# Performance work log

Hardware: AMD Instinct MI355X
Metric: run time of the kernel (lower is better)

Reference implementation:

```python
import jax, jax.numpy as jnp
import numpy as np

N_NODES = 100_000
N_EDGES = 3_200_000
IN_DIM, HID_DIM, EMB_DIM = 128, 64, 32


def setup_inputs() -> dict:
    key = jax.random.key(0)
    k0, k1, k2, k3, k4, k5 = jax.random.split(key, 6)
    x = jax.random.normal(k0, (N_NODES, IN_DIM), dtype=jnp.float32)
    edge_index = jax.random.randint(k1, (2, N_EDGES), 0, N_NODES, dtype=jnp.int32)
    # GCNConv parameters (glorot-ish scale)
    W1 = jax.random.normal(k2, (IN_DIM, HID_DIM), dtype=jnp.float32) / np.sqrt(IN_DIM)
    b1 = jnp.zeros((HID_DIM,), dtype=jnp.float32)
    W2 = jax.random.normal(k3, (HID_DIM, EMB_DIM), dtype=jnp.float32) / np.sqrt(HID_DIM)
    b2 = jnp.zeros((EMB_DIM,), dtype=jnp.float32)
    return {"x": x, "W1": W1, "b1": b1, "W2": W2, "b2": b2, "edge_index": edge_index}


def reference(x, W1, b1, W2, b2, edge_index):
    """Two-layer GCN encoder (PyG GCNConv semantics, eval mode so dropout is a no-op).

    Each GCNConv: add self-loops, symmetric deg^-1/2 normalization,
    out = scatter_add(norm_e * (x @ W)[src], dst) + b.
    """
    N = x.shape[0]
    loops = jnp.arange(N, dtype=edge_index.dtype)
    src = jnp.concatenate([edge_index[0], loops])  # [E+N]
    dst = jnp.concatenate([edge_index[1], loops])  # [E+N]

    # degree of destination nodes (self-loops guarantee deg >= 1)
    deg = jax.ops.segment_sum(jnp.ones_like(dst, dtype=jnp.float32), dst,
                              num_segments=N)
    dinv = jax.lax.rsqrt(deg)                      # deg^-1/2, finite since deg>=1
    norm = dinv[src] * dinv[dst]                   # [E+N]

    def gcn_conv(h, W, b):
        h = h @ W                                  # dense transform [N, D_out]
        msg = h[src] * norm[:, None]               # gather + scale [E+N, D_out]
        return jax.ops.segment_sum(msg, dst, num_segments=N) + b

    h = jax.nn.relu(gcn_conv(x, W1, b1))
    # F.dropout with training=False is identity -> omitted
    return gcn_conv(h, W2, b2)
```

## Files before the change

### kernel.cpp

```cpp
#include <hip/hip_runtime.h>

static constexpr int NN = 100000;
static constexpr int NE = 3200000;
static constexpr int DI = 128;
static constexpr int DH = 64;
static constexpr int DO = 32;

static constexpr int NBK  = 391;
static constexpr int BCAP = 9216;
static constexpr int TILE = 8192;

typedef short short8 __attribute__((ext_vector_type(8)));
typedef float f32x4  __attribute__((ext_vector_type(4)));

__device__ __forceinline__ unsigned short f2bf(float f) {
    union { float f; unsigned u; } v; v.f = f;
    unsigned r = v.u + 0x7FFFu + ((v.u >> 16) & 1u);
    return (unsigned short)(r >> 16);
}
__device__ __forceinline__ float bflo(unsigned u) {
    union { unsigned u; float f; } v; v.u = u << 16; return v.f;
}
__device__ __forceinline__ float bfhi(unsigned u) {
    union { unsigned u; float f; } v; v.u = u & 0xFFFF0000u; return v.f;
}

__global__ void k_zero(int* __restrict__ p, int n) {
    int i = blockIdx.x * blockDim.x + threadIdx.x;
    if (i < n) p[i] = 0;
}

__global__ __launch_bounds__(256) void k_bucket(
        const int* __restrict__ src, const int* __restrict__ dst,
        int* __restrict__ bcur, int* __restrict__ bstore) {
    __shared__ int hist[NBK];
    __shared__ int lcur[NBK];
    __shared__ int gpos[NBK];
    __shared__ int stage[TILE];
    __shared__ unsigned short bid[TILE];

    int tid = threadIdx.x;
    for (int i = tid; i < NBK; i += 256) hist[i] = 0;
    __syncthreads();

    int base = blockIdx.x * TILE;
    int p[32]; unsigned short bb[32];
#pragma unroll
    for (int k = 0; k < 32; ++k) {
        int e = base + k * 256 + tid;
        if (e < NE) {
            int d = dst[e], s = src[e];
            bb[k] = (unsigned short)(d >> 8);
            p[k]  = ((d & 255) << 24) | s;
            atomicAdd(&hist[bb[k]], 1);
        } else bb[k] = 0xFFFF;
    }
    __syncthreads();

    for (int i = tid; i < NBK; i += 256)
        gpos[i] = atomicAdd(&bcur[i], hist[i]);
    __syncthreads();

    if (tid < 64) {
        int carry = 0;
        for (int c = 0; c < (NBK + 63) / 64; ++c) {
            int idx = c * 64 + tid;
            int v = (idx < NBK) ? hist[idx] : 0;
            int inc = v;
#pragma unroll
            for (int o = 1; o < 64; o <<= 1) {
                int u = __shfl_up(inc, o, 64);
                if (tid >= o) inc += u;
            }
            int tot = __shfl(inc, 63, 64);
            if (idx < NBK) { int ex = carry + inc - v; hist[idx] = ex; lcur[idx] = ex; }
            carry += tot;
        }
    }
    __syncthreads();

#pragma unroll
    for (int k = 0; k < 32; ++k) {
        if (bb[k] != 0xFFFF) {
            int lp = atomicAdd(&lcur[bb[k]], 1);
            stage[lp] = p[k];
            bid[lp] = bb[k];
        }
    }
    __syncthreads();

    int tcnt = min(TILE, NE - base);
    for (int i = tid; i < tcnt; i += 256) {
        int b = bid[i];
        int off = gpos[b] + (i - hist[b]);
        if (off < BCAP) bstore[b * BCAP + off] = stage[i];
    }
}

__global__ __launch_bounds__(256) void k_bsort(
        const int* __restrict__ bcur, int* __restrict__ bstore,
        int* __restrict__ rpb, int* __restrict__ rpe, float* __restrict__ dinv) {
    __shared__ int buf[BCAP];
    __shared__ int sorted[BCAP];
    __shared__ int hist[256], scan[256], cur[256];

    int b = blockIdx.x, tid = threadIdx.x;
    int cnt = min(bcur[b], BCAP);
    int base = b * BCAP;
    for (int i = tid; i < cnt; i += 256) buf[i] = bstore[base + i];
    hist[tid] = 0;
    __syncthreads();
    for (int i = tid; i < cnt; i += 256)
        atomicAdd(&hist[((unsigned)buf[i]) >> 24], 1);
    __syncthreads();

    if (tid < 64) {
        int carry = 0;
        for (int c = 0; c < 4; ++c) {
            int idx = c * 64 + tid;
            int v = hist[idx];
            int inc = v;
#pragma unroll
            for (int o = 1; o < 64; o <<= 1) {
                int u = __shfl_up(inc, o, 64);
                if (tid >= o) inc += u;
            }
            int tot = __shfl(inc, 63, 64);
            scan[idx] = carry + inc - v;
            cur[idx]  = carry + inc - v;
            carry += tot;
        }
    }
    __syncthreads();

    int n = b * 256 + tid;
    if (n < NN) {
        int beg = base + scan[tid];
        rpb[n] = beg;
        rpe[n] = beg + hist[tid];
        dinv[n] = rsqrtf(1.0f + (float)hist[tid]);
    }

    for (int i = tid; i < cnt; i += 256) {
        unsigned pv = (unsigned)buf[i];
        int pos = atomicAdd(&cur[pv >> 24], 1);
        sorted[pos] = (int)(pv & 0xFFFFFF);
    }
    __syncthreads();
    for (int i = tid; i < cnt; i += 256) bstore[base + i] = sorted[i];
}

__global__ __launch_bounds__(256) void k_cast_x(const float* __restrict__ x,
                                                unsigned* __restrict__ xbf32) {
    int i = blockIdx.x * 256 + threadIdx.x;
    float a = x[(size_t)i * 4 + 0], b = x[(size_t)i * 4 + 1];
    float c = x[(size_t)i * 4 + 2], d = x[(size_t)i * 4 + 3];
    xbf32[(size_t)i * 2 + 0] = (unsigned)f2bf(a) | ((unsigned)f2bf(b) << 16);
    xbf32[(size_t)i * 2 + 1] = (unsigned)f2bf(c) | ((unsigned)f2bf(d) << 16);
}

__global__ __launch_bounds__(256) void k_cast_w(const float* __restrict__ W1,
                                                const float* __restrict__ W2,
                                                unsigned short* __restrict__ w1bf,
                                                unsigned short* __restrict__ w2bf) {
    int tid = threadIdx.x;
    for (int i = tid; i < DI * DH; i += 256) w1bf[i] = f2bf(W1[i]);
    for (int i = tid; i < DH * DO; i += 256) w2bf[i] = f2bf(W2[i]);
}

__global__ __launch_bounds__(256) void k_xw1_mfma(
        const unsigned short* __restrict__ xbf, const unsigned short* __restrict__ w1bf,
        const float* __restrict__ dinv, unsigned short* __restrict__ h1b) {
    int wave = threadIdx.x >> 6, lane = threadIdx.x & 63;
    int q = lane >> 4, m = lane & 15, o0 = wave * 16;
    int nb = blockIdx.x * 64;

    short8 bf[4];
#pragma unroll
    for (int kb = 0; kb < 4; ++kb)
#pragma unroll
        for (int j = 0; j < 8; ++j)
            bf[kb][j] = (short)w1bf[(kb * 32 + q * 8 + j) * DH + o0 + m];

#pragma unroll
    for (int mt = 0; mt < 4; ++mt) {
        int row = nb + mt * 16 + m;
        f32x4 acc = {0.f, 0.f, 0.f, 0.f};
#pragma unroll
        for (int kb = 0; kb < 4; ++kb) {
            short8 a = *(const short8*)(xbf + (size_t)row * DI + kb * 32 + q * 8);
            acc = __builtin_amdgcn_mfma_f32_16x16x32_bf16(a, bf[kb], acc, 0, 0, 0);
        }
#pragma unroll
        for (int r = 0; r < 4; ++r) {
            int n = nb + mt * 16 + q * 4 + r;
            if (n < NN) h1b[(size_t)n * DH + o0 + m] = f2bf(acc[r] * dinv[n]);
        }
    }
}

__global__ __launch_bounds__(256) void k_gather64(
        const int* __restrict__ rpb, const int* __restrict__ rpe,
        const int* __restrict__ csr, const unsigned* __restrict__ h,
        const float* __restrict__ dinv, const float* __restrict__ b1,
        unsigned* __restrict__ tbf) {
    int wave = threadIdx.x >> 6, lane = threadIdx.x & 63;
    int q = lane >> 4, f4 = lane & 15;
    int n = blockIdx.x * 4 + wave;
    int beg = rpb[n], end = rpe[n];

    float s0 = 0.f, s1 = 0.f, s2 = 0.f, s3 = 0.f;
    if (q == 0) {
        uint2 u = *(const uint2*)(h + (size_t)n * 32 + 2 * f4);
        s0 = bflo(u.x); s1 = bfhi(u.x); s2 = bflo(u.y); s3 = bfhi(u.y);
    }
    for (int c = beg; c < end; c += 64) {
        int cnt = min(64, end - c);
        int sidx = (lane < cnt) ? csr[c + lane] : 0;
        int j = 0;
        for (; j + 8 <= cnt; j += 8) {
            int sa = __shfl(sidx, j + q, 64);
            int sb = __shfl(sidx, j + 4 + q, 64);
            uint2 ua = *(const uint2*)(h + (size_t)sa * 32 + 2 * f4);
            uint2 ub = *(const uint2*)(h + (size_t)sb * 32 + 2 * f4);
            s0 += bflo(ua.x); s1 += bfhi(ua.x); s2 += bflo(ua.y); s3 += bfhi(ua.y);
            s0 += bflo(ub.x); s1 += bfhi(ub.x); s2 += bflo(ub.y); s3 += bfhi(ub.y);
        }
        for (; j < cnt; j += 4) {
            int slot = j + q;
            int s = __shfl(sidx, slot, 64);
            if (slot < cnt) {
                uint2 u = *(const uint2*)(h + (size_t)s * 32 + 2 * f4);
                s0 += bflo(u.x); s1 += bfhi(u.x); s2 += bflo(u.y); s3 += bfhi(u.y);
            }
        }
    }
    s0 += __shfl_xor(s0, 32, 64); s1 += __shfl_xor(s1, 32, 64);
    s2 += __shfl_xor(s2, 32, 64); s3 += __shfl_xor(s3, 32, 64);
    s0 += __shfl_xor(s0, 16, 64); s1 += __shfl_xor(s1, 16, 64);
    s2 += __shfl_xor(s2, 16, 64); s3 += __shfl_xor(s3, 16, 64);
    if (q == 0) {
        float dn = dinv[n];
        float t0 = fmaxf(fmaf(s0, dn, b1[4 * f4 + 0]), 0.f);
        float t1 = fmaxf(fmaf(s1, dn, b1[4 * f4 + 1]), 0.f);
        float t2 = fmaxf(fmaf(s2, dn, b1[4 * f4 + 2]), 0.f);
        float t3 = fmaxf(fmaf(s3, dn, b1[4 * f4 + 3]), 0.f);
        uint2 o;
        o.x = (unsigned)f2bf(t0) | ((unsigned)f2bf(t1) << 16);
        o.y = (unsigned)f2bf(t2) | ((unsigned)f2bf(t3) << 16);
        *(uint2*)(tbf + (size_t)n * 32 + 2 * f4) = o;
    }
}

__global__ __launch_bounds__(256) void k_l2_mfma(
        const unsigned short* __restrict__ tbf, const unsigned short* __restrict__ w2bf,
        const float* __restrict__ dinv, unsigned short* __restrict__ h2b) {
    int wave = threadIdx.x >> 6, lane = threadIdx.x & 63;
    int q = lane >> 4, m = lane & 15;
    int o0 = (wave & 1) * 16, mt = wave >> 1;
    int nb = blockIdx.x * 32;

    short8 bf[2];
#pragma unroll
    for (int kb = 0; kb < 2; ++kb)
#pragma unroll
        for (int j = 0; j < 8; ++j)
            bf[kb][j] = (short)w2bf[(kb * 32 + q * 8 + j) * DO + o0 + m];

    int row = nb + mt * 16 + m;
    f32x4 acc = {0.f, 0.f, 0.f, 0.f};
#pragma unroll
    for (int kb = 0; kb < 2; ++kb) {
        short8 a = *(const short8*)(tbf + (size_t)row * DH + kb * 32 + q * 8);
        acc = __builtin_amdgcn_mfma_f32_16x16x32_bf16(a, bf[kb], acc, 0, 0, 0);
    }
#pragma unroll
    for (int r = 0; r < 4; ++r) {
        int n = nb + mt * 16 + q * 4 + r;
        if (n < NN) h2b[(size_t)n * DO + o0 + m] = f2bf(acc[r] * dinv[n]);
    }
}

__global__ __launch_bounds__(256) void k_gather32(
        const int* __restrict__ rpb, const int* __restrict__ rpe,
        const int* __restrict__ csr, const unsigned* __restrict__ h,
        const float* __restrict__ dinv, const float* __restrict__ b2,
        float* __restrict__ out) {
    int wave = threadIdx.x >> 6, lane = threadIdx.x & 63;
    int q = lane >> 3, f4 = lane & 7;
    int n = blockIdx.x * 4 + wave;
    int beg = rpb[n], end = rpe[n];

    float s0 = 0.f, s1 = 0.f, s2 = 0.f, s3 = 0.f;
    if (q == 0) {
        uint2 u = *(const uint2*)(h + (size_t)n * 16 + 2 * f4);
        s0 = bflo(u.x); s1 = bfhi(u.x); s2 = bflo(u.y); s3 = bfhi(u.y);
    }
    for (int c = beg; c < end; c += 64) {
        int cnt = min(64, end - c);
        int sidx = (lane < cnt) ? csr[c + lane] : 0;
        int j = 0;
        for (; j + 16 <= cnt; j += 16) {
            int sa = __shfl(sidx, j + q, 64);
            int sb = __shfl(sidx, j + 8 + q, 64);
            uint2 ua = *(const uint2*)(h + (size_t)sa * 16 + 2 * f4);
            uint2 ub = *(const uint2*)(h + (size_t)sb * 16 + 2 * f4);
            s0 += bflo(ua.x); s1 += bfhi(ua.x); s2 += bflo(ua.y); s3 += bfhi(ua.y);
            s0 += bflo(ub.x); s1 += bfhi(ub.x); s2 += bflo(ub.y); s3 += bfhi(ub.y);
        }
        for (; j < cnt; j += 8) {
            int slot = j + q;
            int s = __shfl(sidx, slot, 64);
            if (slot < cnt) {
                uint2 u = *(const uint2*)(h + (size_t)s * 16 + 2 * f4);
                s0 += bflo(u.x); s1 += bfhi(u.x); s2 += bflo(u.y); s3 += bfhi(u.y);
            }
        }
    }
    s0 += __shfl_xor(s0, 32, 64); s1 += __shfl_xor(s1, 32, 64);
    s2 += __shfl_xor(s2, 32, 64); s3 += __shfl_xor(s3, 32, 64);
    s0 += __shfl_xor(s0, 16, 64); s1 += __shfl_xor(s1, 16, 64);
    s2 += __shfl_xor(s2, 16, 64); s3 += __shfl_xor(s3, 16, 64);
    s0 += __shfl_xor(s0, 8, 64);  s1 += __shfl_xor(s1, 8, 64);
    s2 += __shfl_xor(s2, 8, 64);  s3 += __shfl_xor(s3, 8, 64);
    if (q == 0) {
        float dn = dinv[n];
        size_t o = (size_t)n * 32 + 4 * f4;
        out[o + 0] = fmaf(s0, dn, b2[4 * f4 + 0]);
        out[o + 1] = fmaf(s1, dn, b2[4 * f4 + 1]);
        out[o + 2] = fmaf(s2, dn, b2[4 * f4 + 2]);
        out[o + 3] = fmaf(s3, dn, b2[4 * f4 + 3]);
    }
}

extern "C" void kernel_launch(void* const* d_in, const int* in_sizes, int n_in,
                              void* d_out, int out_size, void* d_ws, size_t ws_size,
                              hipStream_t stream) {
    const float* x  = (const float*)d_in[0];
    const float* W1 = (const float*)d_in[1];
    const float* b1 = (const float*)d_in[2];
    const float* W2 = (const float*)d_in[3];
    const float* b2 = (const float*)d_in[4];
    const int* ei  = (const int*)d_in[5];
    const int* src = ei;
    const int* dst = ei + NE;
    float* out = (float*)d_out;

    float* ws    = (float*)d_ws;
    int*   rpb   = (int*)ws;
    int*   rpe   = (int*)(ws + 100352);
    float* dinv  = ws + 200704;
    int*   bcur  = (int*)(ws + 301056);
    int*   bstor = (int*)(ws + 301568);
    unsigned short* w1bf = (unsigned short*)(ws + 3905024);
    unsigned short* w2bf = (unsigned short*)(ws + 3909120);
    unsigned short* xbf  = (unsigned short*)(ws + 3910144);
    unsigned short* tbf  = xbf;
    unsigned short* h1b  = (unsigned short*)(ws + 10332672);
    unsigned short* h2b  = h1b;

    k_zero     <<<2, 256, 0, stream>>>(bcur, 512);
    k_bucket   <<<(NE + TILE - 1) / TILE, 256, 0, stream>>>(src, dst, bcur, bstor);
    k_bsort    <<<NBK, 256, 0, stream>>>(bcur, bstor, rpb, rpe, dinv);

    k_cast_x   <<<NN * DI / 4 / 256, 256, 0, stream>>>(x, (unsigned*)xbf);
    k_cast_w   <<<1, 256, 0, stream>>>(W1, W2, w1bf, w2bf);

    k_xw1_mfma <<<(NN + 63) / 64, 256, 0, stream>>>(xbf, w1bf, dinv, h1b);
    k_gather64 <<<NN / 4, 256, 0, stream>>>(rpb, rpe, bstor, (const unsigned*)h1b,
                                            dinv, b1, (unsigned*)tbf);
    k_l2_mfma  <<<NN / 32, 256, 0, stream>>>(tbf, w2bf, dinv, h2b);
    k_gather32 <<<NN / 4, 256, 0, stream>>>(rpb, rpe, bstor, (const unsigned*)h2b,
                                            dinv, b2, out);
}
```

Before: 295.1 us.

## Fuse bucketing, weight cast and X·W1 into one launch; scale by dinv in gather

Merges the edge bucketing kernel, the W2 cast, and the X·W1 MFMA (now reading fp32 x and W1 directly and converting in registers) into a single heterogeneous launch. This removes the separate x-cast pass and its bf16 round trip through memory, and lets the matmul overlap with bucketing. Because dinv is not yet known when h1 is computed, the source-side dinv scaling moves into the layer-1 gather as an extra per-edge dinv load. k_bsort also goes to 512 threads per block. The cost is an extra random 4-byte load per edge in the gather and larger shared-memory blocks running alongside the matmul blocks.

Measured after the change: 274.7 us. -6.9%, faster.

```diff
diff --git a/kernel.cpp b/kernel.cpp
--- a/kernel.cpp
+++ b/kernel.cpp
@@ -9,6 +9,8 @@
 static constexpr int NBK  = 391;
 static constexpr int BCAP = 9216;
 static constexpr int TILE = 8192;
+static constexpr int XW1_BASE = 392;
+static constexpr int XW1_BLOCKS = (NN + 63) / 64;
 
 typedef short short8 __attribute__((ext_vector_type(8)));
 typedef float f32x4  __attribute__((ext_vector_type(4)));
@@ -30,9 +32,12 @@
     if (i < n) p[i] = 0;
 }
 
-__global__ __launch_bounds__(256) void k_bucket(
+__global__ __launch_bounds__(256) void k_mega(
         const int* __restrict__ src, const int* __restrict__ dst,
-        int* __restrict__ bcur, int* __restrict__ bstore) {
+        int* __restrict__ bcur, int* __restrict__ bstore,
+        const float* __restrict__ x, const float* __restrict__ W1,
+        const float* __restrict__ W2,
+        unsigned short* __restrict__ w2bf, unsigned short* __restrict__ h1b) {
     __shared__ int hist[NBK];
     __shared__ int lcur[NBK];
     __shared__ int gpos[NBK];
@@ -40,64 +45,103 @@
     __shared__ unsigned short bid[TILE];
 
     int tid = threadIdx.x;
-    for (int i = tid; i < NBK; i += 256) hist[i] = 0;
-    __syncthreads();
-
-    int base = blockIdx.x * TILE;
-    int p[32]; unsigned short bb[32];
-#pragma unroll
-    for (int k = 0; k < 32; ++k) {
-        int e = base + k * 256 + tid;
-        if (e < NE) {
-            int d = dst[e], s = src[e];
-            bb[k] = (unsigned short)(d >> 8);
-            p[k]  = ((d & 255) << 24) | s;
-            atomicAdd(&hist[bb[k]], 1);
-        } else bb[k] = 0xFFFF;
-    }
-    __syncthreads();
-
-    for (int i = tid; i < NBK; i += 256)
-        gpos[i] = atomicAdd(&bcur[i], hist[i]);
-    __syncthreads();
-
-    if (tid < 64) {
-        int carry = 0;
-        for (int c = 0; c < (NBK + 63) / 64; ++c) {
-            int idx = c * 64 + tid;
-            int v = (idx < NBK) ? hist[idx] : 0;
-            int inc = v;
-#pragma unroll
-            for (int o = 1; o < 64; o <<= 1) {
-                int u = __shfl_up(inc, o, 64);
-                if (tid >= o) inc += u;
-            }
-            int tot = __shfl(inc, 63, 64);
-            if (idx < NBK) { int ex = carry + inc - v; hist[idx] = ex; lcur[idx] = ex; }
-            carry += tot;
-        }
-    }
-    __syncthreads();
-
-#pragma unroll
-    for (int k = 0; k < 32; ++k) {
-        if (bb[k] != 0xFFFF) {
-            int lp = atomicAdd(&lcur[bb[k]], 1);
-            stage[lp] = p[k];
-            bid[lp] = bb[k];
-        }
-    }
-    __syncthreads();
-
-    int tcnt = min(TILE, NE - base);
-    for (int i = tid; i < tcnt; i += 256) {
-        int b = bid[i];
-        int off = gpos[b] + (i - hist[b]);
-        if (off < BCAP) bstore[b * BCAP + off] = stage[i];
-    }
-}
-
-__global__ __launch_bounds__(256) void k_bsort(
+
+    if (blockIdx.x < NBK) {
+        for (int i = tid; i < NBK; i += 256) hist[i] = 0;
+        __syncthreads();
+
+        int base = blockIdx.x * TILE;
+        int p[32]; unsigned short bb[32];
+#pragma unroll
+        for (int k = 0; k < 32; ++k) {
+            int e = base + k * 256 + tid;
+            if (e < NE) {
+                int d = dst[e], s = src[e];
+                bb[k] = (unsigned short)(d >> 8);
+                p[k]  = ((d & 255) << 24) | s;
+                atomicAdd(&hist[bb[k]], 1);
+            } else bb[k] = 0xFFFF;
+        }
+        __syncthreads();
+
+        for (int i = tid; i < NBK; i += 256)
+            gpos[i] = atomicAdd(&bcur[i], hist[i]);
+        __syncthreads();
+
+        if (tid < 64) {
+            int carry = 0;
+            for (int c = 0; c < (NBK + 63) / 64; ++c) {
+                int idx = c * 64 + tid;
+                int v = (idx < NBK) ? hist[idx] : 0;
+                int inc = v;
+#pragma unroll
+                for (int o = 1; o < 64; o <<= 1) {
+                    int u = __shfl_up(inc, o, 64);
+                    if (tid >= o) inc += u;
+                }
+                int tot = __shfl(inc, 63, 64);
+                if (idx < NBK) { int ex = carry + inc - v; hist[idx] = ex; lcur[idx] = ex; }
+                carry += tot;
+            }
+        }
+        __syncthreads();
+
+#pragma unroll
+        for (int k = 0; k < 32; ++k) {
+            if (bb[k] != 0xFFFF) {
+                int lp = atomicAdd(&lcur[bb[k]], 1);
+                stage[lp] = p[k];
+                bid[lp] = bb[k];
+            }
+        }
+        __syncthreads();
+
+        int tcnt = min(TILE, NE - base);
+        for (int i = tid; i < tcnt; i += 256) {
+            int b = bid[i];
+            int off = gpos[b] + (i - hist[b]);
+            if (off < BCAP) bstore[b * BCAP + off] = stage[i];
+        }
+    } else if (blockIdx.x == NBK) {
+        for (int i = tid; i < DH * DO; i += 256) w2bf[i] = f2bf(W2[i]);
+    } else {
+        int wave = tid >> 6, lane = tid & 63;
+        int q = lane >> 4, m = lane & 15, o0 = wave * 16;
+        int nb = (blockIdx.x - XW1_BASE) * 64;
+
+        short8 bfr[4];
+#pragma unroll
+        for (int kb = 0; kb < 4; ++kb)
+#pragma unroll
+            for (int j = 0; j < 8; ++j)
+                bfr[kb][j] = (short)f2bf(W1[(kb * 32 + q * 8 + j) * DH + o0 + m]);
+
+#pragma unroll
+        for (int mt = 0; mt < 4; ++mt) {
+            int row = min(nb + mt * 16 + m, NN - 1);
+            const float* xr = x + (size_t)row * DI;
+            f32x4 acc = {0.f, 0.f, 0.f, 0.f};
+#pragma unroll
+            for (int kb = 0; kb < 4; ++kb) {
+                f32x4 u0 = *(const f32x4*)(xr + kb * 32 + q * 8);
+                f32x4 u1 = *(const f32x4*)(xr + kb * 32 + q * 8 + 4);
+                short8 a;
+                a[0] = (short)f2bf(u0.x); a[1] = (short)f2bf(u0.y);
+                a[2] = (short)f2bf(u0.z); a[3] = (short)f2bf(u0.w);
+                a[4] = (short)f2bf(u1.x); a[5] = (short)f2bf(u1.y);
+                a[6] = (short)f2bf(u1.z); a[7] = (short)f2bf(u1.w);
+                acc = __builtin_amdgcn_mfma_f32_16x16x32_bf16(a, bfr[kb], acc, 0, 0, 0);
+            }
+#pragma unroll
+            for (int r = 0; r < 4; ++r) {
+                int n = nb + mt * 16 + q * 4 + r;
+                if (n < NN) h1b[(size_t)n * DH + o0 + m] = f2bf(acc[r]);
+            }
+        }
+    }
+}
+
+__global__ __launch_bounds__(512) void k_bsort(
         const int* __restrict__ bcur, int* __restrict__ bstore,
         int* __restrict__ rpb, int* __restrict__ rpe, float* __restrict__ dinv) {
     __shared__ int buf[BCAP];
@@ -107,10 +151,10 @@
     int b = blockIdx.x, tid = threadIdx.x;
     int cnt = min(bcur[b], BCAP);
     int base = b * BCAP;
-    for (int i = tid; i < cnt; i += 256) buf[i] = bstore[base + i];
-    hist[tid] = 0;
+    for (int i = tid; i < cnt; i += 512) buf[i] = bstore[base + i];
+    if (tid < 256) hist[tid] = 0;
     __syncthreads();
-    for (int i = tid; i < cnt; i += 256)
+    for (int i = tid; i < cnt; i += 512)
         atomicAdd(&hist[((unsigned)buf[i]) >> 24], 1);
     __syncthreads();
 
@@ -133,70 +177,23 @@
     }
     __syncthreads();
 
-    int n = b * 256 + tid;
-    if (n < NN) {
-        int beg = base + scan[tid];
-        rpb[n] = beg;
-        rpe[n] = beg + hist[tid];
-        dinv[n] = rsqrtf(1.0f + (float)hist[tid]);
-    }
-
-    for (int i = tid; i < cnt; i += 256) {
+    if (tid < 256) {
+        int n = b * 256 + tid;
+        if (n < NN) {
+            int beg = base + scan[tid];
+            rpb[n] = beg;
+            rpe[n] = beg + hist[tid];
+            dinv[n] = rsqrtf(1.0f + (float)hist[tid]);
+        }
+    }
+
+    for (int i = tid; i < cnt; i += 512) {
         unsigned pv = (unsigned)buf[i];
         int pos = atomicAdd(&cur[pv >> 24], 1);
         sorted[pos] = (int)(pv & 0xFFFFFF);
     }
     __syncthreads();
-    for (int i = tid; i < cnt; i += 256) bstore[base + i] = sorted[i];
-}
-
-__global__ __launch_bounds__(256) void k_cast_x(const float* __restrict__ x,
-                                                unsigned* __restrict__ xbf32) {
-    int i = blockIdx.x * 256 + threadIdx.x;
-    float a = x[(size_t)i * 4 + 0], b = x[(size_t)i * 4 + 1];
-    float c = x[(size_t)i * 4 + 2], d = x[(size_t)i * 4 + 3];
-    xbf32[(size_t)i * 2 + 0] = (unsigned)f2bf(a) | ((unsigned)f2bf(b) << 16);
-    xbf32[(size_t)i * 2 + 1] = (unsigned)f2bf(c) | ((unsigned)f2bf(d) << 16);
-}
-
-__global__ __launch_bounds__(256) void k_cast_w(const float* __restrict__ W1,
-                                                const float* __restrict__ W2,
-                                                unsigned short* __restrict__ w1bf,
-                                                unsigned short* __restrict__ w2bf) {
-    int tid = threadIdx.x;
-    for (int i = tid; i < DI * DH; i += 256) w1bf[i] = f2bf(W1[i]);
-    for (int i = tid; i < DH * DO; i += 256) w2bf[i] = f2bf(W2[i]);
-}
-
-__global__ __launch_bounds__(256) void k_xw1_mfma(
-        const unsigned short* __restrict__ xbf, const unsigned short* __restrict__ w1bf,
-        const float* __restrict__ dinv, unsigned short* __restrict__ h1b) {
-    int wave = threadIdx.x >> 6, lane = threadIdx.x & 63;
-    int q = lane >> 4, m = lane & 15, o0 = wave * 16;
-    int nb = blockIdx.x * 64;
-
-    short8 bf[4];
-#pragma unroll
-    for (int kb = 0; kb < 4; ++kb)
-#pragma unroll
-        for (int j = 0; j < 8; ++j)
-            bf[kb][j] = (short)w1bf[(kb * 32 + q * 8 + j) * DH + o0 + m];
-
-#pragma unroll
-    for (int mt = 0; mt < 4; ++mt) {
-        int row = nb + mt * 16 + m;
-        f32x4 acc = {0.f, 0.f, 0.f, 0.f};
-#pragma unroll
-        for (int kb = 0; kb < 4; ++kb) {
-            short8 a = *(const short8*)(xbf + (size_t)row * DI + kb * 32 + q * 8);
-            acc = __builtin_amdgcn_mfma_f32_16x16x32_bf16(a, bf[kb], acc, 0, 0, 0);
-        }
-#pragma unroll
-        for (int r = 0; r < 4; ++r) {
-            int n = nb + mt * 16 + q * 4 + r;
-            if (n < NN) h1b[(size_t)n * DH + o0 + m] = f2bf(acc[r] * dinv[n]);
-        }
-    }
+    for (int i = tid; i < cnt; i += 512) bstore[base + i] = sorted[i];
 }
 
 __global__ __launch_bounds__(256) void k_gather64(
@@ -208,11 +205,13 @@
     int q = lane >> 4, f4 = lane & 15;
     int n = blockIdx.x * 4 + wave;
     int beg = rpb[n], end = rpe[n];
+    float dn = dinv[n];
 
     float s0 = 0.f, s1 = 0.f, s2 = 0.f, s3 = 0.f;
     if (q == 0) {
         uint2 u = *(const uint2*)(h + (size_t)n * 32 + 2 * f4);
-        s0 = bflo(u.x); s1 = bfhi(u.x); s2 = bflo(u.y); s3 = bfhi(u.y);
+        s0 = bflo(u.x) * dn; s1 = bfhi(u.x) * dn;
+        s2 = bflo(u.y) * dn; s3 = bfhi(u.y) * dn;
     }
     for (int c = beg; c < end; c += 64) {
         int cnt = min(64, end - c);
@@ -221,17 +220,22 @@
         for (; j + 8 <= cnt; j += 8) {
             int sa = __shfl(sidx, j + q, 64);
             int sb = __shfl(sidx, j + 4 + q, 64);
+            float da = dinv[sa], db = dinv[sb];
             uint2 ua = *(const uint2*)(h + (size_t)sa * 32 + 2 * f4);
             uint2 ub = *(const uint2*)(h + (size_t)sb * 32 + 2 * f4);
-            s0 += bflo(ua.x); s1 += bfhi(ua.x); s2 += bflo(ua.y); s3 += bfhi(ua.y);
-            s0 += bflo(ub.x); s1 += bfhi(ub.x); s2 += bflo(ub.y); s3 += bfhi(ub.y);
+            s0 = fmaf(bflo(ua.x), da, s0); s1 = fmaf(bfhi(ua.x), da, s1);
+            s2 = fmaf(bflo(ua.y), da, s2); s3 = fmaf(bfhi(ua.y), da, s3);
+            s0 = fmaf(bflo(ub.x), db, s0); s1 = fmaf(bfhi(ub.x), db, s1);
+            s2 = fmaf(bflo(ub.y), db, s2); s3 = fmaf(bfhi(ub.y), db, s3);
         }
         for (; j < cnt; j += 4) {
             int slot = j + q;
             int s = __shfl(sidx, slot, 64);
             if (slot < cnt) {
+                float dv = dinv[s];
                 uint2 u = *(const uint2*)(h + (size_t)s * 32 + 2 * f4);
-                s0 += bflo(u.x); s1 += bfhi(u.x); s2 += bflo(u.y); s3 += bfhi(u.y);
+                s0 = fmaf(bflo(u.x), dv, s0); s1 = fmaf(bfhi(u.x), dv, s1);
+                s2 = fmaf(bflo(u.y), dv, s2); s3 = fmaf(bfhi(u.y), dv, s3);
             }
         }
     }
@@ -240,7 +244,6 @@
     s0 += __shfl_xor(s0, 16, 64); s1 += __shfl_xor(s1, 16, 64);
     s2 += __shfl_xor(s2, 16, 64); s3 += __shfl_xor(s3, 16, 64);
     if (q == 0) {
-        float dn = dinv[n];
         float t0 = fmaxf(fmaf(s0, dn, b1[4 * f4 + 0]), 0.f);
         float t1 = fmaxf(fmaf(s1, dn, b1[4 * f4 + 1]), 0.f);
         float t2 = fmaxf(fmaf(s2, dn, b1[4 * f4 + 2]), 0.f);
@@ -352,21 +355,16 @@
     float* dinv  = ws + 200704;
     int*   bcur  = (int*)(ws + 301056);
     int*   bstor = (int*)(ws + 301568);
-    unsigned short* w1bf = (unsigned short*)(ws + 3905024);
-    unsigned short* w2bf = (unsigned short*)(ws + 3909120);
-    unsigned short* xbf  = (unsigned short*)(ws + 3910144);
-    unsigned short* tbf  = xbf;
-    unsigned short* h1b  = (unsigned short*)(ws + 10332672);
+    unsigned short* w2bf = (unsigned short*)(ws + 3905024);
+    unsigned short* tbf  = (unsigned short*)(ws + 3906048);
+    unsigned short* h1b  = (unsigned short*)(ws + 7106048);
     unsigned short* h2b  = h1b;
 
     k_zero     <<<2, 256, 0, stream>>>(bcur, 512);
-    k_bucket   <<<(NE + TILE - 1) / TILE, 256, 0, stream>>>(src, dst, bcur, bstor);
-    k_bsort    <<<NBK, 256, 0, stream>>>(bcur, bstor, rpb, rpe, dinv);
-
-    k_cast_x   <<<NN * DI / 4 / 256, 256, 0, stream>>>(x, (unsigned*)xbf);
-    k_cast_w   <<<1, 256, 0, stream>>>(W1, W2, w1bf, w2bf);
-
-    k_xw1_mfma <<<(NN + 63) / 64, 256, 0, stream>>>(xbf, w1bf, dinv, h1b);
+    k_mega     <<<XW1_BASE + XW1_BLOCKS, 256, 0, stream>>>(
+                    src, dst, bcur, bstor, x, W1, W2, w2bf, h1b);
+    k_bsort    <<<NBK, 512, 0, stream>>>(bcur, bstor, rpb, rpe, dinv);
+
     k_gather64 <<<NN / 4, 256, 0, stream>>>(rpb, rpe, bstor, (const unsigned*)h1b,
                                             dinv, b1, (unsigned*)tbf);
     k_l2_mfma  <<<NN / 32, 256, 0, stream>>>(tbf, w2bf, dinv, h2b);
```
